# Performance work log

Hardware: AMD Instinct MI355X
Metric: run time of the kernel (lower is better)

Reference implementation:

```python
import jax, jax.numpy as jnp
import numpy as np

B, L, D = 2, 384, 128
N, DHS, DHP = 8, 16, 4  # heads, scalar head dim, point head dim
D_SCALAR = N * DHS          # 128
D_POINT = N * DHP * 3       # 96
D_OUT_IN = D_SCALAR + D * N + D_POINT + N * DHP  # 1280


def setup_inputs() -> dict:
    key = jax.random.key(0)
    ks = jax.random.split(key, 14)
    sc = 0.05
    x = jax.random.normal(ks[0], (B, L, D), dtype=jnp.float32)
    e = jax.random.normal(ks[1], (B, L, L, D), dtype=jnp.float32)
    r = jax.random.normal(ks[2], (B, L, 3, 3), dtype=jnp.float32)
    t = jax.random.normal(ks[3], (B, L, 3), dtype=jnp.float32)
    Wq_s = jax.random.normal(ks[4], (D, D_SCALAR)) * sc
    Wk_s = jax.random.normal(ks[5], (D, D_SCALAR)) * sc
    Wv_s = jax.random.normal(ks[6], (D, D_SCALAR)) * sc
    Wb = jax.random.normal(ks[7], (D, N)) * sc
    Wq_p = jax.random.normal(ks[8], (D, D_POINT)) * sc
    Wk_p = jax.random.normal(ks[9], (D, D_POINT)) * sc
    Wv_p = jax.random.normal(ks[10], (D, D_POINT)) * sc
    gamma = jnp.full((N,), float(np.log(np.exp(1.0) - 1.0)), dtype=jnp.float32)
    Wo = jax.random.normal(ks[11], (D_OUT_IN, D)) * sc
    bo = jnp.zeros((D,), dtype=jnp.float32)
    return {"x": x, "e": e, "r": r, "t": t, "Wq_s": Wq_s, "Wk_s": Wk_s,
            "Wv_s": Wv_s, "Wb": Wb, "Wq_p": Wq_p, "Wk_p": Wk_p,
            "Wv_p": Wv_p, "gamma": gamma, "Wo": Wo, "bo": bo}


def _heads_scalar(y):  # (b,l,n*d) -> (b,n,l,d)
    b, l, _ = y.shape
    return y.reshape(b, l, N, DHS).transpose(0, 2, 1, 3)


def _heads_point(y):  # (b,l,n*p*3) -> (b,n,l,p,3)
    b, l, _ = y.shape
    return y.reshape(b, l, N, DHP, 3).transpose(0, 2, 1, 3, 4)


def reference(x, e, r, t, Wq_s, Wk_s, Wv_s, Wb, Wq_p, Wk_p, Wv_p, gamma, Wo, bo):
    b, l, _ = x.shape
    qs = _heads_scalar(x @ Wq_s)
    ks_ = _heads_scalar(x @ Wk_s)
    vs = _heads_scalar(x @ Wv_s)

    # local points -> global frame: x_row @ r + t (note row-vector convention)
    t_b = t[:, None, :, None, :]  # (b,1,l,1,3)
    qp = jnp.einsum('bnlpk,blkc->bnlpc', _heads_point(x @ Wq_p), r) + t_b
    kp = jnp.einsum('bnlpk,blkc->bnlpc', _heads_point(x @ Wk_p), r) + t_b
    vp = jnp.einsum('bnlpk,blkc->bnlpc', _heads_point(x @ Wv_p), r) + t_b

    logit_scalar = jnp.einsum('bnid,bnjd->bnij', qs, ks_) * (DHS ** -0.5)
    bias_pair = jnp.einsum('bijd,dn->bnij', e, Wb)

    # sum_{p,c} (q_i - k_j)^2 via norm expansion (same math, no O(l^2 p 3) tensor)
    qq = jnp.sum(qp * qp, axis=(-1, -2))  # (b,n,i)
    kk = jnp.sum(kp * kp, axis=(-1, -2))  # (b,n,j)
    cross = jnp.einsum('bnipc,bnjpc->bnij', qp, kp)
    dist2 = qq[..., :, None] + kk[..., None, :] - 2.0 * cross
    logit_point = (-0.5 * 0.25) * gamma[None, :, None, None] * dist2

    logit = (3.0 ** -0.5) * (logit_scalar + bias_pair + logit_point)
    attn = jax.nn.softmax(logit, axis=-1)  # (b,n,i,j)

    out_scalar = jnp.einsum('bnij,bnjd->bnid', attn, vs)
    out_scalar = out_scalar.transpose(0, 2, 1, 3).reshape(b, l, N * DHS)

    out_pair = jnp.einsum('bnij,bijd->bnid', attn, e)
    out_pair = out_pair.transpose(0, 2, 1, 3).reshape(b, l, N * D)

    op = jnp.einsum('bnij,bnjpc->bnipc', attn, vp)
    # inverse transform: (x - t) @ r^T  -> out[c] = sum_k (x-t)[k] * r[c,k]
    op_local = jnp.einsum('bnipk,bick->bnipc', op - t_b, r)
    op_norm = jnp.linalg.norm(op_local, axis=-1)  # (b,n,i,p)

    out_point = op_local.transpose(0, 2, 1, 3, 4).reshape(b, l, N * DHP * 3)
    out_norm = op_norm.transpose(0, 2, 1, 3).reshape(b, l, N * DHP)

    out = jnp.concatenate([out_scalar, out_pair, out_point, out_norm], axis=-1)
    return out @ Wo + bo
```

## Files before the change

### kernel.cpp

```cpp
#include <hip/hip_runtime.h>
#include <hip/hip_bf16.h>

#define BB 2
#define LL 384
#define DD 128
#define NH 8

typedef const float* fp32p;

__global__ __launch_bounds__(128) void k_proj(
    fp32p x, fp32p r, fp32p tvec,
    fp32p Wqs, fp32p Wks, fp32p Wvs,
    fp32p Wqp, fp32p Wkp, fp32p Wvp,
    float* qs, float* ks, float* vs,
    float* qp, float* kp, float* vp)
{
  int bl = blockIdx.x;
  int t = threadIdx.x;
  __shared__ float xs[128];
  __shared__ float yq[96], yk[96], yv[96];
  xs[t] = x[bl*128 + t];
  __syncthreads();
  float aq = 0.f, ak = 0.f, av = 0.f;
  for (int d = 0; d < 128; ++d) {
    float xv = xs[d];
    aq += xv * Wqs[d*128 + t];
    ak += xv * Wks[d*128 + t];
    av += xv * Wvs[d*128 + t];
  }
  int b = bl / LL, l = bl - (bl / LL) * LL;
  int n = t >> 4, dhs = t & 15;
  int rowbase = (b*NH + n)*LL + l;
  qs[rowbase*16 + dhs] = aq;
  ks[rowbase*16 + dhs] = ak;
  vs[rowbase*16 + dhs] = av;
  if (t < 96) {
    float pq = 0.f, pk = 0.f, pv = 0.f;
    for (int d = 0; d < 128; ++d) {
      float xv = xs[d];
      pq += xv * Wqp[d*96 + t];
      pk += xv * Wkp[d*96 + t];
      pv += xv * Wvp[d*96 + t];
    }
    yq[t] = pq; yk[t] = pk; yv[t] = pv;
  }
  __syncthreads();
  if (t < 96) {
    int np = t / 12;
    int rem = t - np*12;
    int p = rem / 3, c = rem - p*3;
    float rr0 = r[(bl*3 + 0)*3 + c];
    float rr1 = r[(bl*3 + 1)*3 + c];
    float rr2 = r[(bl*3 + 2)*3 + c];
    float tt  = tvec[bl*3 + c];
    int base = np*12 + p*3;
    int prow = (b*NH + np)*LL + l;
    qp[prow*12 + p*3 + c] = yq[base]*rr0 + yq[base+1]*rr1 + yq[base+2]*rr2 + tt;
    kp[prow*12 + p*3 + c] = yk[base]*rr0 + yk[base+1]*rr1 + yk[base+2]*rr2 + tt;
    vp[prow*12 + p*3 + c] = yv[base]*rr0 + yv[base+1]*rr1 + yv[base+2]*rr2 + tt;
  }
}

__global__ __launch_bounds__(256) void k_bias(fp32p e, fp32p Wb, float* bias)
{
  __shared__ float WbS[128*8];
  for (int idx = threadIdx.x; idx < 1024; idx += 256) WbS[idx] = Wb[idx];
  __syncthreads();
  int tid = blockIdx.x*256 + threadIdx.x;
  int b = tid / (LL*LL);
  int rem = tid - b*(LL*LL);
  int i = rem / LL, j = rem - (rem / LL)*LL;
  const float4* erow = reinterpret_cast<const float4*>(e) + (size_t)tid * 32;
  float acc[8] = {0,0,0,0,0,0,0,0};
  for (int it = 0; it < 32; ++it) {
    float4 v4 = erow[it];
    float vv[4] = {v4.x, v4.y, v4.z, v4.w};
    #pragma unroll
    for (int k = 0; k < 4; ++k) {
      float v = vv[k];
      const float* wr = &WbS[(it*4 + k)*8];
      #pragma unroll
      for (int nn = 0; nn < 8; ++nn) acc[nn] += v * wr[nn];
    }
  }
  #pragma unroll
  for (int nn = 0; nn < 8; ++nn)
    bias[(((size_t)(b*NH + nn)*LL + i)*LL) + j] = acc[nn];
}

__global__ __launch_bounds__(256) void k_attn(
    const float* qs, const float* ks, const float* qp, const float* kp,
    fp32p gamma, float* attn)
{
  int row = blockIdx.x*4 + (threadIdx.x >> 6);
  int lane = threadIdx.x & 63;
  int bn = row / LL;
  int n = bn & 7;
  int rowbase = bn * LL;
  float q[16];
  const float4* q4 = reinterpret_cast<const float4*>(qs + (size_t)row*16);
  #pragma unroll
  for (int k2 = 0; k2 < 4; ++k2) { float4 v = q4[k2]; q[4*k2]=v.x; q[4*k2+1]=v.y; q[4*k2+2]=v.z; q[4*k2+3]=v.w; }
  float qpv[12];
  const float4* p4 = reinterpret_cast<const float4*>(qp + (size_t)row*12);
  #pragma unroll
  for (int k2 = 0; k2 < 3; ++k2) { float4 v = p4[k2]; qpv[4*k2]=v.x; qpv[4*k2+1]=v.y; qpv[4*k2+2]=v.z; qpv[4*k2+3]=v.w; }
  float qq = 0.f;
  #pragma unroll
  for (int k2 = 0; k2 < 12; ++k2) qq += qpv[k2]*qpv[k2];
  float coef = -0.125f * gamma[n];
  float lg[6];
  float* arow = attn + (size_t)row*LL;
  #pragma unroll
  for (int jj = 0; jj < 6; ++jj) {
    int j = lane + jj*64;
    const float4* k4 = reinterpret_cast<const float4*>(ks + (size_t)(rowbase + j)*16);
    float dots = 0.f;
    #pragma unroll
    for (int k2 = 0; k2 < 4; ++k2) { float4 v = k4[k2]; dots += q[4*k2]*v.x + q[4*k2+1]*v.y + q[4*k2+2]*v.z + q[4*k2+3]*v.w; }
    const float4* kp4 = reinterpret_cast<const float4*>(kp + (size_t)(rowbase + j)*12);
    float cross = 0.f, kk = 0.f;
    #pragma unroll
    for (int k2 = 0; k2 < 3; ++k2) {
      float4 v = kp4[k2];
      cross += qpv[4*k2]*v.x + qpv[4*k2+1]*v.y + qpv[4*k2+2]*v.z + qpv[4*k2+3]*v.w;
      kk += v.x*v.x + v.y*v.y + v.z*v.z + v.w*v.w;
    }
    float bs = arow[j];
    lg[jj] = 0.57735027f * (0.25f*dots + bs + coef*(qq + kk - 2.f*cross));
  }
  float m = lg[0];
  #pragma unroll
  for (int jj = 1; jj < 6; ++jj) m = fmaxf(m, lg[jj]);
  #pragma unroll
  for (int off = 32; off >= 1; off >>= 1) m = fmaxf(m, __shfl_xor(m, off, 64));
  float el[6]; float s = 0.f;
  #pragma unroll
  for (int jj = 0; jj < 6; ++jj) { el[jj] = __expf(lg[jj] - m); s += el[jj]; }
  #pragma unroll
  for (int off = 32; off >= 1; off >>= 1) s += __shfl_xor(s, off, 64);
  float inv = 1.f / s;
  #pragma unroll
  for (int jj = 0; jj < 6; ++jj) arow[lane + jj*64] = el[jj]*inv;
}

__global__ __launch_bounds__(256) void k_av(
    const float* attn, const float* vs, const float* vp, float* cat, float* opb)
{
  int tid = blockIdx.x*256 + threadIdx.x;
  int row = tid >> 5;
  int dim = tid & 31;
  if (dim >= 28) return;
  int i = row % LL;
  int bn = row / LL;
  int rowbase = bn * LL;
  const float* arow = attn + (size_t)row*LL;
  const float* src; int stride;
  if (dim < 16) { src = vs + (size_t)rowbase*16 + dim; stride = 16; }
  else          { src = vp + (size_t)rowbase*12 + (dim - 16); stride = 12; }
  float acc = 0.f;
  for (int j = 0; j < LL; ++j) acc += arow[j] * src[(size_t)j*stride];
  int b = bn >> 3, n = bn & 7;
  if (dim < 16) cat[((size_t)(b*LL + i))*1280 + n*16 + dim] = acc;
  else          opb[(size_t)row*12 + (dim - 16)] = acc;
}

__global__ __launch_bounds__(256) void k_pair(fp32p e, const float* attn, float* cat)
{
  int bi = blockIdx.x;
  int b = bi / LL, i = bi - (bi / LL)*LL;
  __shared__ float attnS[8*384];
  __shared__ float redS[128*9];
  for (int idx = threadIdx.x; idx < 8*384; idx += 256) {
    int n = idx / 384, j = idx - n*384;
    attnS[idx] = attn[(((size_t)(b*NH + n)*LL + i)*LL) + j];
  }
  __syncthreads();
  int t = threadIdx.x;
  int oct = t & 15;
  int n = (t >> 4) & 7;
  int half = t >> 7;
  const float4* ebase = reinterpret_cast<const float4*>(e) + (size_t)bi*LL*32;
  const float* an = attnS + n*384;
  float acc[8] = {0,0,0,0,0,0,0,0};
  for (int jj = 0; jj < 192; ++jj) {
    int j = 2*jj + half;
    float4 va = ebase[j*32 + oct*2];
    float4 vb = ebase[j*32 + oct*2 + 1];
    float a = an[j];
    acc[0] += a * va.x; acc[1] += a * va.y; acc[2] += a * va.z; acc[3] += a * va.w;
    acc[4] += a * vb.x; acc[5] += a * vb.y; acc[6] += a * vb.z; acc[7] += a * vb.w;
  }
  if (half) {
    #pragma unroll
    for (int k = 0; k < 8; ++k) redS[(t - 128)*9 + k] = acc[k];
  }
  __syncthreads();
  if (!half) {
    float* dst = cat + (size_t)bi*1280 + 128 + n*128 + oct*8;
    #pragma unroll
    for (int k = 0; k < 8; ++k) dst[k] = acc[k] + redS[t*9 + k];
  }
}

__global__ __launch_bounds__(256) void k_pt(const float* opb, fp32p r, fp32p tvec, float* cat)
{
  int tid = blockIdx.x*256 + threadIdx.x;
  int p = tid & 3;
  int row = tid >> 2;
  int i = row % LL;
  int bn = row / LL;
  int b = bn >> 3, n = bn & 7;
  int bi = b*LL + i;
  float o[3];
  #pragma unroll
  for (int k = 0; k < 3; ++k)
    o[k] = opb[(size_t)row*12 + p*3 + k] - tvec[bi*3 + k];
  float loc[3];
  #pragma unroll
  for (int c = 0; c < 3; ++c) {
    float s = 0.f;
    #pragma unroll
    for (int k = 0; k < 3; ++k) s += o[k] * r[(bi*3 + c)*3 + k];
    loc[c] = s;
  }
  float* dst = cat + (size_t)bi*1280;
  dst[1152 + n*12 + p*3 + 0] = loc[0];
  dst[1152 + n*12 + p*3 + 1] = loc[1];
  dst[1152 + n*12 + p*3 + 2] = loc[2];
  dst[1248 + n*4 + p] = sqrtf(loc[0]*loc[0] + loc[1]*loc[1] + loc[2]*loc[2]);
}

__global__ __launch_bounds__(128) void k_out(const float* cat, fp32p Wo, fp32p bo,
                                             float* out)
{
  __shared__ float catS[4*1280];
  int row0 = blockIdx.x*4;
  for (int idx = threadIdx.x; idx < 4*1280; idx += 128)
    catS[idx] = cat[(size_t)row0*1280 + idx];
  __syncthreads();
  int t = threadIdx.x;
  float bov = bo[t];
  float a0 = bov, a1 = bov, a2 = bov, a3 = bov;
  for (int k = 0; k < 1280; ++k) {
    float w = Wo[k*128 + t];
    a0 += catS[k]        * w;
    a1 += catS[1280 + k] * w;
    a2 += catS[2560 + k] * w;
    a3 += catS[3840 + k] * w;
  }
  out[(size_t)(row0 + 0)*128 + t] = a0;
  out[(size_t)(row0 + 1)*128 + t] = a1;
  out[(size_t)(row0 + 2)*128 + t] = a2;
  out[(size_t)(row0 + 3)*128 + t] = a3;
}

extern "C" void kernel_launch(void* const* d_in, const int* in_sizes, int n_in,
                              void* d_out, int out_size, void* d_ws, size_t ws_size,
                              hipStream_t stream)
{
  fp32p x    = (fp32p)d_in[0];
  fp32p e    = (fp32p)d_in[1];
  fp32p r    = (fp32p)d_in[2];
  fp32p tv   = (fp32p)d_in[3];
  fp32p Wqs  = (fp32p)d_in[4];
  fp32p Wks  = (fp32p)d_in[5];
  fp32p Wvs  = (fp32p)d_in[6];
  fp32p Wb   = (fp32p)d_in[7];
  fp32p Wqp  = (fp32p)d_in[8];
  fp32p Wkp  = (fp32p)d_in[9];
  fp32p Wvp  = (fp32p)d_in[10];
  fp32p gam  = (fp32p)d_in[11];
  fp32p Wo   = (fp32p)d_in[12];
  fp32p bo   = (fp32p)d_in[13];
  float* out = (float*)d_out;

  float* qs   = (float*)d_ws;
  float* ks   = qs + 98304;
  float* vs   = ks + 98304;
  float* qp   = vs + 98304;
  float* kp   = qp + 73728;
  float* vp   = kp + 73728;
  float* attn = vp + 73728;
  float* opb  = attn + 2359296;
  float* cat  = opb + 73728;

  k_proj<<<768, 128, 0, stream>>>(x, r, tv, Wqs, Wks, Wvs, Wqp, Wkp, Wvp,
                                  qs, ks, vs, qp, kp, vp);
  k_bias<<<1152, 256, 0, stream>>>(e, Wb, attn);
  k_attn<<<1536, 256, 0, stream>>>(qs, ks, qp, kp, gam, attn);
  k_av<<<768, 256, 0, stream>>>(attn, vs, vp, cat, opb);
  k_pair<<<768, 256, 0, stream>>>(e, attn, cat);
  k_pt<<<96, 256, 0, stream>>>(opb, r, tv, cat);
  k_out<<<192, 128, 0, stream>>>(cat, Wo, bo, out);
}
```

Baseline: 422.7 us.

## Fuse attention softmax, AV and pair aggregation into one kernel per query row

```diff
diff --git a/kernel.cpp b/kernel.cpp
--- a/kernel.cpp
+++ b/kernel.cpp
@@ -1,5 +1,4 @@
 #include <hip/hip_runtime.h>
-#include <hip/hip_bf16.h>
 
 #define BB 2
 #define LL 384
@@ -63,24 +62,21 @@
 
 __global__ __launch_bounds__(256) void k_bias(fp32p e, fp32p Wb, float* bias)
 {
-  __shared__ float WbS[128*8];
-  for (int idx = threadIdx.x; idx < 1024; idx += 256) WbS[idx] = Wb[idx];
-  __syncthreads();
   int tid = blockIdx.x*256 + threadIdx.x;
   int b = tid / (LL*LL);
   int rem = tid - b*(LL*LL);
   int i = rem / LL, j = rem - (rem / LL)*LL;
   const float4* erow = reinterpret_cast<const float4*>(e) + (size_t)tid * 32;
   float acc[8] = {0,0,0,0,0,0,0,0};
+  #pragma unroll
   for (int it = 0; it < 32; ++it) {
     float4 v4 = erow[it];
     float vv[4] = {v4.x, v4.y, v4.z, v4.w};
     #pragma unroll
     for (int k = 0; k < 4; ++k) {
       float v = vv[k];
-      const float* wr = &WbS[(it*4 + k)*8];
       #pragma unroll
-      for (int nn = 0; nn < 8; ++nn) acc[nn] += v * wr[nn];
+      for (int nn = 0; nn < 8; ++nn) acc[nn] += v * Wb[(it*4 + k)*8 + nn];
     }
   }
   #pragma unroll
@@ -88,36 +84,52 @@
     bias[(((size_t)(b*NH + nn)*LL + i)*LL) + j] = acc[nn];
 }
 
-__global__ __launch_bounds__(256) void k_attn(
-    const float* qs, const float* ks, const float* qp, const float* kp,
-    fp32p gamma, float* attn)
-{
-  int row = blockIdx.x*4 + (threadIdx.x >> 6);
-  int lane = threadIdx.x & 63;
-  int bn = row / LL;
-  int n = bn & 7;
-  int rowbase = bn * LL;
-  float q[16];
-  const float4* q4 = reinterpret_cast<const float4*>(qs + (size_t)row*16);
-  #pragma unroll
-  for (int k2 = 0; k2 < 4; ++k2) { float4 v = q4[k2]; q[4*k2]=v.x; q[4*k2+1]=v.y; q[4*k2+2]=v.z; q[4*k2+3]=v.w; }
-  float qpv[12];
-  const float4* p4 = reinterpret_cast<const float4*>(qp + (size_t)row*12);
-  #pragma unroll
-  for (int k2 = 0; k2 < 3; ++k2) { float4 v = p4[k2]; qpv[4*k2]=v.x; qpv[4*k2+1]=v.y; qpv[4*k2+2]=v.z; qpv[4*k2+3]=v.w; }
+__global__ __launch_bounds__(256) void k_fused(
+    const float* __restrict__ qs, const float* __restrict__ ks,
+    const float* __restrict__ vs, const float* __restrict__ qp,
+    const float* __restrict__ kp, const float* __restrict__ vp,
+    const float* __restrict__ bias, fp32p gamma, fp32p e,
+    float* __restrict__ cat, float* __restrict__ opb)
+{
+  __shared__ float eS[64*128];
+  __shared__ float lgS[NH*LL];
+  __shared__ float sS[NH];
+
+  int bi = blockIdx.x;
+  int b = bi / LL, i = bi - (bi / LL)*LL;
+  int t = threadIdx.x;
+  int n = t >> 5, l32 = t & 31;
+
+  const float4* e4 = reinterpret_cast<const float4*>(e) + (size_t)bi * (LL*DD/4);
+  float4 stg[8];
+  #pragma unroll
+  for (int rd = 0; rd < 8; ++rd) stg[rd] = e4[rd*256 + t];
+
+  int rowq = (b*NH + n)*LL + i;
+  int rowbase = (b*NH + n)*LL;
+  float q[16], qpv[12];
+  {
+    const float4* q4 = reinterpret_cast<const float4*>(qs + (size_t)rowq*16);
+    #pragma unroll
+    for (int k2 = 0; k2 < 4; ++k2) { float4 v = q4[k2]; q[4*k2]=v.x; q[4*k2+1]=v.y; q[4*k2+2]=v.z; q[4*k2+3]=v.w; }
+    const float4* p4 = reinterpret_cast<const float4*>(qp + (size_t)rowq*12);
+    #pragma unroll
+    for (int k2 = 0; k2 < 3; ++k2) { float4 v = p4[k2]; qpv[4*k2]=v.x; qpv[4*k2+1]=v.y; qpv[4*k2+2]=v.z; qpv[4*k2+3]=v.w; }
+  }
   float qq = 0.f;
   #pragma unroll
   for (int k2 = 0; k2 < 12; ++k2) qq += qpv[k2]*qpv[k2];
   float coef = -0.125f * gamma[n];
-  float lg[6];
-  float* arow = attn + (size_t)row*LL;
-  #pragma unroll
-  for (int jj = 0; jj < 6; ++jj) {
-    int j = lane + jj*64;
+  const float* brow = bias + (size_t)rowq*LL;
+  for (int jj = 0; jj < 12; ++jj) {
+    int j = l32 + jj*32;
     const float4* k4 = reinterpret_cast<const float4*>(ks + (size_t)(rowbase + j)*16);
     float dots = 0.f;
     #pragma unroll
-    for (int k2 = 0; k2 < 4; ++k2) { float4 v = k4[k2]; dots += q[4*k2]*v.x + q[4*k2+1]*v.y + q[4*k2+2]*v.z + q[4*k2+3]*v.w; }
+    for (int k2 = 0; k2 < 4; ++k2) {
+      float4 v = k4[k2];
+      dots += q[4*k2]*v.x + q[4*k2+1]*v.y + q[4*k2+2]*v.z + q[4*k2+3]*v.w;
+    }
     const float4* kp4 = reinterpret_cast<const float4*>(kp + (size_t)(rowbase + j)*12);
     float cross = 0.f, kk = 0.f;
     #pragma unroll
@@ -126,81 +138,61 @@
       cross += qpv[4*k2]*v.x + qpv[4*k2+1]*v.y + qpv[4*k2+2]*v.z + qpv[4*k2+3]*v.w;
       kk += v.x*v.x + v.y*v.y + v.z*v.z + v.w*v.w;
     }
-    float bs = arow[j];
-    lg[jj] = 0.57735027f * (0.25f*dots + bs + coef*(qq + kk - 2.f*cross));
-  }
-  float m = lg[0];
-  #pragma unroll
-  for (int jj = 1; jj < 6; ++jj) m = fmaxf(m, lg[jj]);
-  #pragma unroll
-  for (int off = 32; off >= 1; off >>= 1) m = fmaxf(m, __shfl_xor(m, off, 64));
-  float el[6]; float s = 0.f;
-  #pragma unroll
-  for (int jj = 0; jj < 6; ++jj) { el[jj] = __expf(lg[jj] - m); s += el[jj]; }
-  #pragma unroll
-  for (int off = 32; off >= 1; off >>= 1) s += __shfl_xor(s, off, 64);
-  float inv = 1.f / s;
-  #pragma unroll
-  for (int jj = 0; jj < 6; ++jj) arow[lane + jj*64] = el[jj]*inv;
-}
-
-__global__ __launch_bounds__(256) void k_av(
-    const float* attn, const float* vs, const float* vp, float* cat, float* opb)
-{
-  int tid = blockIdx.x*256 + threadIdx.x;
-  int row = tid >> 5;
-  int dim = tid & 31;
-  if (dim >= 28) return;
-  int i = row % LL;
-  int bn = row / LL;
-  int rowbase = bn * LL;
-  const float* arow = attn + (size_t)row*LL;
-  const float* src; int stride;
-  if (dim < 16) { src = vs + (size_t)rowbase*16 + dim; stride = 16; }
-  else          { src = vp + (size_t)rowbase*12 + (dim - 16); stride = 12; }
-  float acc = 0.f;
-  for (int j = 0; j < LL; ++j) acc += arow[j] * src[(size_t)j*stride];
-  int b = bn >> 3, n = bn & 7;
-  if (dim < 16) cat[((size_t)(b*LL + i))*1280 + n*16 + dim] = acc;
-  else          opb[(size_t)row*12 + (dim - 16)] = acc;
-}
-
-__global__ __launch_bounds__(256) void k_pair(fp32p e, const float* attn, float* cat)
-{
-  int bi = blockIdx.x;
-  int b = bi / LL, i = bi - (bi / LL)*LL;
-  __shared__ float attnS[8*384];
-  __shared__ float redS[128*9];
-  for (int idx = threadIdx.x; idx < 8*384; idx += 256) {
-    int n = idx / 384, j = idx - n*384;
-    attnS[idx] = attn[(((size_t)(b*NH + n)*LL + i)*LL) + j];
-  }
-  __syncthreads();
-  int t = threadIdx.x;
-  int oct = t & 15;
-  int n = (t >> 4) & 7;
-  int half = t >> 7;
-  const float4* ebase = reinterpret_cast<const float4*>(e) + (size_t)bi*LL*32;
-  const float* an = attnS + n*384;
-  float acc[8] = {0,0,0,0,0,0,0,0};
-  for (int jj = 0; jj < 192; ++jj) {
-    int j = 2*jj + half;
-    float4 va = ebase[j*32 + oct*2];
-    float4 vb = ebase[j*32 + oct*2 + 1];
-    float a = an[j];
-    acc[0] += a * va.x; acc[1] += a * va.y; acc[2] += a * va.z; acc[3] += a * va.w;
-    acc[4] += a * vb.x; acc[5] += a * vb.y; acc[6] += a * vb.z; acc[7] += a * vb.w;
-  }
-  if (half) {
-    #pragma unroll
-    for (int k = 0; k < 8; ++k) redS[(t - 128)*9 + k] = acc[k];
-  }
-  __syncthreads();
-  if (!half) {
-    float* dst = cat + (size_t)bi*1280 + 128 + n*128 + oct*8;
-    #pragma unroll
-    for (int k = 0; k < 8; ++k) dst[k] = acc[k] + redS[t*9 + k];
-  }
+    lgS[n*LL + j] = 0.57735027f * (0.25f*dots + brow[j] + coef*(qq + kk - 2.f*cross));
+  }
+  __syncthreads();
+
+  int wv = t >> 6, ln = t & 63;
+  for (int nn = wv; nn < 8; nn += 4) {
+    float v[6]; float m = -1e30f;
+    #pragma unroll
+    for (int k2 = 0; k2 < 6; ++k2) { v[k2] = lgS[nn*LL + ln + 64*k2]; m = fmaxf(m, v[k2]); }
+    #pragma unroll
+    for (int off = 32; off >= 1; off >>= 1) m = fmaxf(m, __shfl_xor(m, off, 64));
+    float s = 0.f;
+    #pragma unroll
+    for (int k2 = 0; k2 < 6; ++k2) { float p = __expf(v[k2] - m); s += p; lgS[nn*LL + ln + 64*k2] = p; }
+    #pragma unroll
+    for (int off = 32; off >= 1; off >>= 1) s += __shfl_xor(s, off, 64);
+    if (ln == 0) sS[nn] = s;
+  }
+
+  float4 pacc = {0.f, 0.f, 0.f, 0.f};
+  float sacc = 0.f;
+  const float* pn = lgS + n*LL;
+  const float* vrow0; int vstr;
+  if (l32 < 16) { vrow0 = vs + (size_t)rowbase*16 + l32; vstr = 16; }
+  else { int comp = (l32 < 28) ? (l32 - 16) : 0; vrow0 = vp + (size_t)rowbase*12 + comp; vstr = 12; }
+
+  for (int tile = 0; tile < 6; ++tile) {
+    __syncthreads();
+    float4* eW = reinterpret_cast<float4*>(eS);
+    #pragma unroll
+    for (int rd = 0; rd < 8; ++rd) eW[rd*256 + t] = stg[rd];
+    __syncthreads();
+    if (tile < 5) {
+      #pragma unroll
+      for (int rd = 0; rd < 8; ++rd) stg[rd] = e4[(tile+1)*2048 + rd*256 + t];
+    }
+    const float* pt0 = pn + tile*64;
+    const float* vrow = vrow0 + (size_t)tile*64*vstr;
+    #pragma unroll 4
+    for (int jj = 0; jj < 64; ++jj) {
+      float a = pt0[jj];
+      float4 ev = *reinterpret_cast<const float4*>(eS + jj*128 + l32*4);
+      pacc.x += a*ev.x; pacc.y += a*ev.y; pacc.z += a*ev.z; pacc.w += a*ev.w;
+      float vvl = vrow[(size_t)jj*vstr];
+      sacc += a * vvl;
+    }
+  }
+
+  float inv = 1.f / sS[n];
+  float* cbase = cat + (size_t)bi*1280;
+  if (l32 < 16)       cbase[n*16 + l32] = sacc * inv;
+  else if (l32 < 28)  opb[(size_t)rowq*12 + (l32 - 16)] = sacc * inv;
+  float4 pw;
+  pw.x = pacc.x*inv; pw.y = pacc.y*inv; pw.z = pacc.z*inv; pw.w = pacc.w*inv;
+  *reinterpret_cast<float4*>(cbase + 128 + n*128 + l32*4) = pw;
 }
 
 __global__ __launch_bounds__(256) void k_pt(const float* opb, fp32p r, fp32p tvec, float* cat)
@@ -231,28 +223,30 @@
   dst[1248 + n*4 + p] = sqrtf(loc[0]*loc[0] + loc[1]*loc[1] + loc[2]*loc[2]);
 }
 
-__global__ __launch_bounds__(128) void k_out(const float* cat, fp32p Wo, fp32p bo,
+__global__ __launch_bounds__(256) void k_out(const float* cat, fp32p Wo, fp32p bo,
                                              float* out)
 {
-  __shared__ float catS[4*1280];
-  int row0 = blockIdx.x*4;
-  for (int idx = threadIdx.x; idx < 4*1280; idx += 128)
+  __shared__ float catS[2*1280];
+  __shared__ float red[2*128];
+  int row0 = blockIdx.x*2;
+  for (int idx = threadIdx.x; idx < 2*1280; idx += 256)
     catS[idx] = cat[(size_t)row0*1280 + idx];
   __syncthreads();
-  int t = threadIdx.x;
-  float bov = bo[t];
-  float a0 = bov, a1 = bov, a2 = bov, a3 = bov;
-  for (int k = 0; k < 1280; ++k) {
-    float w = Wo[k*128 + t];
+  int col = threadIdx.x & 127, half = threadIdx.x >> 7;
+  float a0 = 0.f, a1 = 0.f;
+  int k0 = half*640;
+  for (int k = k0; k < k0 + 640; ++k) {
+    float w = Wo[k*128 + col];
     a0 += catS[k]        * w;
     a1 += catS[1280 + k] * w;
-    a2 += catS[2560 + k] * w;
-    a3 += catS[3840 + k] * w;
-  }
-  out[(size_t)(row0 + 0)*128 + t] = a0;
-  out[(size_t)(row0 + 1)*128 + t] = a1;
-  out[(size_t)(row0 + 2)*128 + t] = a2;
-  out[(size_t)(row0 + 3)*128 + t] = a3;
+  }
+  if (half) { red[col] = a0; red[128 + col] = a1; }
+  __syncthreads();
+  if (!half) {
+    float bv = bo[col];
+    out[(size_t)(row0 + 0)*128 + col] = a0 + red[col]       + bv;
+    out[(size_t)(row0 + 1)*128 + col] = a1 + red[128 + col] + bv;
+  }
 }
 
 extern "C" void kernel_launch(void* const* d_in, const int* in_sizes, int n_in,
@@ -281,16 +275,14 @@
   float* qp   = vs + 98304;
   float* kp   = qp + 73728;
   float* vp   = kp + 73728;
-  float* attn = vp + 73728;
-  float* opb  = attn + 2359296;
+  float* bias = vp + 73728;
+  float* opb  = bias + 2359296;
   float* cat  = opb + 73728;
 
   k_proj<<<768, 128, 0, stream>>>(x, r, tv, Wqs, Wks, Wvs, Wqp, Wkp, Wvp,
                                   qs, ks, vs, qp, kp, vp);
-  k_bias<<<1152, 256, 0, stream>>>(e, Wb, attn);
-  k_attn<<<1536, 256, 0, stream>>>(qs, ks, qp, kp, gam, attn);
-  k_av<<<768, 256, 0, stream>>>(attn, vs, vp, cat, opb);
-  k_pair<<<768, 256, 0, stream>>>(e, attn, cat);
+  k_bias<<<1152, 256, 0, stream>>>(e, Wb, bias);
+  k_fused<<<768, 256, 0, stream>>>(qs, ks, vs, qp, kp, vp, bias, gam, e, cat, opb);
   k_pt<<<96, 256, 0, stream>>>(opb, r, tv, cat);
-  k_out<<<192, 128, 0, stream>>>(cat, Wo, bo, out);
-}
+  k_out<<<384, 256, 0, stream>>>(cat, Wo, bo, out);
+}
```

Result: faster. 400.8 us (-5.2%).
